# Performance work log

Measured on AMD Instinct MI355X. Metric: run time of the kernel, lower is better.

## Reference

```python
import jax, jax.numpy as jnp
import numpy as np

N = 500_000          # number of tree nodes
K = 8                # attributes per group
ROWS, COLS = 2048, 4096   # image size; P = ROWS*COLS pixels


def _build_euler_tour(n, seed=0):
    """Random tree (parent[i] < i, parent[0] = 0) + real DFS Euler tour with a
    single timer incremented on both entry (tpre) and exit (tpost)."""
    rng = np.random.default_rng(seed)
    parent = np.zeros(n, dtype=np.int64)
    if n > 1:
        parent[1:] = np.floor(rng.random(n - 1) * np.arange(1, n)).astype(np.int64)
    counts = np.bincount(parent[1:], minlength=n)
    starts = np.zeros(n, dtype=np.int64)
    starts[1:] = np.cumsum(counts)[:-1]
    child_order = np.argsort(parent[1:], kind='stable') + 1  # children grouped by parent
    tpre = np.empty(n, dtype=np.int64)
    tpost = np.empty(n, dtype=np.int64)
    next_child = starts.copy()
    ends = starts + counts
    stack = np.empty(n, dtype=np.int64)
    sp = 0
    stack[0] = 0
    timer = 0
    tpre[0] = timer; timer += 1
    while sp >= 0:
        u = stack[sp]
        if next_child[u] < ends[u]:
            v = child_order[next_child[u]]
            next_child[u] += 1
            sp += 1
            stack[sp] = v
            tpre[v] = timer; timer += 1
        else:
            tpost[u] = timer; timer += 1
            sp -= 1
    return tpre, tpost


def setup_inputs() -> dict:
    key = jax.random.key(0)
    k1, k2, k3, k4 = jax.random.split(key, 4)
    tpre_np, tpost_np = _build_euler_tour(N)
    weight = jax.random.normal(k1, (K,), dtype=jnp.float32) * 0.1
    bias = jnp.zeros((1,), dtype=jnp.float32)
    residues = jax.random.normal(k2, (N,), dtype=jnp.float32)
    attrs2d = jax.random.uniform(k3, (N, K), dtype=jnp.float32)
    node_of_pixel = jax.random.randint(k4, (ROWS * COLS,), 0, N)
    return {
        'weight': weight,
        'bias': bias,
        'residues': residues,
        'attrs2d': attrs2d,
        'tpre': jnp.asarray(tpre_np),
        'tpost': jnp.asarray(tpost_np),
        'node_of_pixel': node_of_pixel,
        'numRows': ROWS,
        'numCols': COLS,
    }


def reference(weight, bias, residues, attrs2d, tpre, tpost, node_of_pixel, numRows, numCols):
    beta_f = 1.0  # module default; clamp_logits=False
    # logits = attrs2d @ w + b ; filtered residues per node
    logits = attrs2d @ weight + bias[0]                     # (N,)
    sig = jax.nn.sigmoid(beta_f * logits)                   # (N,)
    filtered = residues * sig                                # (N,)
    # implicit J.T @ filtered via Euler-tour scatter + prefix scan
    T = 2 * tpre.shape[0]                                    # tpost.max()+1 for a full DFS tour
    delta = (jnp.zeros((T,), dtype=filtered.dtype)
             .at[tpre].add(filtered)
             .at[tpost].add(-filtered))
    y_cumsum = jnp.cumsum(delta)                             # (2N,)
    y = y_cumsum[tpre[node_of_pixel]]                        # (P,) gather per pixel
    return y.reshape(numRows, numCols)
```

## Files before the change

### kernel.cpp

```cpp
#include <hip/hip_runtime.h>

#define SCAN_THREADS 256
#define EPT 8
#define CHUNK (SCAN_THREADS * EPT)

__global__ void k1_filter_scatter(const float* __restrict__ attrs,
                                  const float* __restrict__ weight,
                                  const float* __restrict__ bias,
                                  const float* __restrict__ residues,
                                  const int* __restrict__ tpre,
                                  const int* __restrict__ tpost,
                                  float* __restrict__ delta,
                                  int N) {
    int u = blockIdx.x * blockDim.x + threadIdx.x;
    if (u >= N) return;
    const float4* a4 = (const float4*)(attrs + (size_t)u * 8);
    float4 a0 = a4[0];
    float4 a1 = a4[1];
    float4 w0 = ((const float4*)weight)[0];
    float4 w1 = ((const float4*)weight)[1];
    float logit = a0.x * w0.x + a0.y * w0.y + a0.z * w0.z + a0.w * w0.w +
                  a1.x * w1.x + a1.y * w1.y + a1.z * w1.z + a1.w * w1.w +
                  bias[0];
    float sig = 1.0f / (1.0f + __expf(-logit));
    float f = residues[u] * sig;
    delta[tpre[u]]  =  f;
    delta[tpost[u]] = -f;
}

__global__ void k2_partials(const float* __restrict__ delta,
                            float* __restrict__ partials, int T) {
    __shared__ float sdata[SCAN_THREADS / 64];
    int base = blockIdx.x * CHUNK + threadIdx.x * EPT;
    float s = 0.0f;
    if (base + EPT <= T) {
        float4 v0 = *(const float4*)(delta + base);
        float4 v1 = *(const float4*)(delta + base + 4);
        s = v0.x + v0.y + v0.z + v0.w + v1.x + v1.y + v1.z + v1.w;
    } else {
        for (int i = 0; i < EPT; ++i)
            if (base + i < T) s += delta[base + i];
    }
    for (int d = 32; d > 0; d >>= 1) s += __shfl_down(s, d, 64);
    int lane = threadIdx.x & 63, wid = threadIdx.x >> 6;
    if (lane == 0) sdata[wid] = s;
    __syncthreads();
    if (threadIdx.x == 0) {
        float tot = 0.0f;
        for (int i = 0; i < SCAN_THREADS / 64; ++i) tot += sdata[i];
        partials[blockIdx.x] = tot;
    }
}

__global__ void k3_scan_partials(const float* __restrict__ partials,
                                 float* __restrict__ offsets, int numChunks) {
    int lane = threadIdx.x;
    int ppl = (numChunks + 63) >> 6;
    float s = 0.0f;
    for (int i = 0; i < ppl; ++i) {
        int idx = lane * ppl + i;
        if (idx < numChunks) s += partials[idx];
    }
    float x = s;
    for (int d = 1; d < 64; d <<= 1) {
        float y = __shfl_up(x, d, 64);
        if (lane >= d) x += y;
    }
    float run = x - s;
    for (int i = 0; i < ppl; ++i) {
        int idx = lane * ppl + i;
        if (idx < numChunks) { offsets[idx] = run; run += partials[idx]; }
    }
}

__global__ void k4_scan_chunks(float* __restrict__ data,
                               const float* __restrict__ offsets, int T) {
    __shared__ float wavesums[SCAN_THREADS / 64];
    int base = blockIdx.x * CHUNK + threadIdx.x * EPT;
    float v[EPT];
    bool full = (base + EPT <= T);
    if (full) {
        float4 v0 = *(const float4*)(data + base);
        float4 v1 = *(const float4*)(data + base + 4);
        v[0] = v0.x; v[1] = v0.y; v[2] = v0.z; v[3] = v0.w;
        v[4] = v1.x; v[5] = v1.y; v[6] = v1.z; v[7] = v1.w;
    } else {
        for (int i = 0; i < EPT; ++i)
            v[i] = (base + i < T) ? data[base + i] : 0.0f;
    }
    float run = 0.0f;
    for (int i = 0; i < EPT; ++i) { run += v[i]; v[i] = run; }
    float tot = run;
    int lane = threadIdx.x & 63, wid = threadIdx.x >> 6;
    float x = tot;
    for (int d = 1; d < 64; d <<= 1) {
        float y = __shfl_up(x, d, 64);
        if (lane >= d) x += y;
    }
    if (lane == 63) wavesums[wid] = x;
    __syncthreads();
    float woff = 0.0f;
    for (int i = 0; i < wid; ++i) woff += wavesums[i];
    float add = (x - tot) + woff + offsets[blockIdx.x];
    if (full) {
        float4 o0 = make_float4(v[0] + add, v[1] + add, v[2] + add, v[3] + add);
        float4 o1 = make_float4(v[4] + add, v[5] + add, v[6] + add, v[7] + add);
        *(float4*)(data + base)     = o0;
        *(float4*)(data + base + 4) = o1;
    } else {
        for (int i = 0; i < EPT; ++i)
            if (base + i < T) data[base + i] = v[i] + add;
    }
}

__global__ void k5_node_values(const float* __restrict__ ycum,
                               const int* __restrict__ tpre,
                               float* __restrict__ vnode, int N) {
    int u = blockIdx.x * blockDim.x + threadIdx.x;
    if (u < N) vnode[u] = ycum[tpre[u]];
}

__global__ void k6_gather(const float* __restrict__ vnode,
                          const int* __restrict__ nop,
                          float* __restrict__ out, int P) {
    int i = (blockIdx.x * blockDim.x + threadIdx.x) * 4;
    if (i + 4 <= P) {
        int4 n = *(const int4*)(nop + i);
        float4 o = make_float4(vnode[n.x], vnode[n.y], vnode[n.z], vnode[n.w]);
        *(float4*)(out + i) = o;
    } else {
        for (; i < P; ++i) out[i] = vnode[nop[i]];
    }
}

__global__ void k6_direct(const float* __restrict__ ycum,
                          const int* __restrict__ tpre,
                          const int* __restrict__ nop,
                          float* __restrict__ out, int P) {
    int i = (blockIdx.x * blockDim.x + threadIdx.x) * 4;
    if (i + 4 <= P) {
        int4 n = *(const int4*)(nop + i);
        float4 o = make_float4(ycum[tpre[n.x]], ycum[tpre[n.y]],
                               ycum[tpre[n.z]], ycum[tpre[n.w]]);
        *(float4*)(out + i) = o;
    } else {
        for (; i < P; ++i) out[i] = ycum[tpre[nop[i]]];
    }
}

extern "C" void kernel_launch(void* const* d_in, const int* in_sizes, int n_in,
                              void* d_out, int out_size, void* d_ws, size_t ws_size,
                              hipStream_t stream) {
    const float* weight   = (const float*)d_in[0];
    const float* bias     = (const float*)d_in[1];
    const float* residues = (const float*)d_in[2];
    const float* attrs    = (const float*)d_in[3];
    const int*   tpre     = (const int*)d_in[4];
    const int*   tpost    = (const int*)d_in[5];
    const int*   nop      = (const int*)d_in[6];
    float* out = (float*)d_out;

    const int N = in_sizes[2];
    const int T = 2 * N;
    const int P = out_size;
    const int numChunks = (T + CHUNK - 1) / CHUNK;

    size_t needFull = (size_t)(T + N + 2 * 1024) * sizeof(float);
    size_t needMid  = (size_t)(N + 2 * 1024) * sizeof(float);

    float* delta;
    float* vnode    = nullptr;
    float* partials;
    float* offsets;
    bool useVnode = true;

    if (ws_size >= needFull) {
        delta    = (float*)d_ws;
        vnode    = delta + T;
        partials = vnode + N;
        offsets  = partials + 1024;
    } else if (ws_size >= needMid) {
        delta    = out;
        vnode    = (float*)d_ws;
        partials = vnode + N;
        offsets  = partials + 1024;
    } else {
        delta    = out;
        partials = (float*)d_ws;
        offsets  = partials + 1024;
        useVnode = false;
    }

    k1_filter_scatter<<<(N + 255) / 256, 256, 0, stream>>>(
        attrs, weight, bias, residues, tpre, tpost, delta, N);
    k2_partials<<<numChunks, SCAN_THREADS, 0, stream>>>(delta, partials, T);
    k3_scan_partials<<<1, 64, 0, stream>>>(partials, offsets, numChunks);
    k4_scan_chunks<<<numChunks, SCAN_THREADS, 0, stream>>>(delta, offsets, T);

    int gatherBlocks = (P / 4 + 255) / 256;
    if (useVnode) {
        k5_node_values<<<(N + 255) / 256, 256, 0, stream>>>(delta, tpre, vnode, N);
        k6_gather<<<gatherBlocks, 256, 0, stream>>>(vnode, nop, out, P);
    } else {
        k6_direct<<<gatherBlocks, 256, 0, stream>>>(delta, tpre, nop, out, P);
    }
}
```

Before: 166.3 us.

## Replace three-kernel scan with single-pass decoupled-lookback scan and widen per-thread work

The separate partials, partial-scan and chunk-scan kernels become one single-pass scan. Each tile takes a dynamic ticket, publishes its aggregate or inclusive prefix as a flag-packed 64-bit word, and looks back over earlier tiles one wavefront at a time. This removes two launches and one full extra pass over the delta buffer. In exchange it adds a memset for the control state and spin-waits on earlier tiles. The filter/scatter, node-value and pixel-gather kernels are also widened to 4, 8 and 16 elements per thread, with nontemporal loads and stores on the streaming arrays, to raise memory-level parallelism.

```diff
diff --git a/kernel.cpp b/kernel.cpp
--- a/kernel.cpp
+++ b/kernel.cpp
@@ -3,6 +3,13 @@
 #define SCAN_THREADS 256
 #define EPT 8
 #define CHUNK (SCAN_THREADS * EPT)
+
+typedef int   v4i __attribute__((ext_vector_type(4)));
+typedef float v4f __attribute__((ext_vector_type(4)));
+
+__device__ inline unsigned long long pack_sf(float v, unsigned flag) {
+    return ((unsigned long long)flag << 32) | (unsigned long long)__float_as_uint(v);
+}
 
 __global__ void k1_filter_scatter(const float* __restrict__ attrs,
                                   const float* __restrict__ weight,
@@ -12,101 +19,133 @@
                                   const int* __restrict__ tpost,
                                   float* __restrict__ delta,
                                   int N) {
-    int u = blockIdx.x * blockDim.x + threadIdx.x;
-    if (u >= N) return;
-    const float4* a4 = (const float4*)(attrs + (size_t)u * 8);
-    float4 a0 = a4[0];
-    float4 a1 = a4[1];
-    float4 w0 = ((const float4*)weight)[0];
-    float4 w1 = ((const float4*)weight)[1];
-    float logit = a0.x * w0.x + a0.y * w0.y + a0.z * w0.z + a0.w * w0.w +
-                  a1.x * w1.x + a1.y * w1.y + a1.z * w1.z + a1.w * w1.w +
-                  bias[0];
-    float sig = 1.0f / (1.0f + __expf(-logit));
-    float f = residues[u] * sig;
-    delta[tpre[u]]  =  f;
-    delta[tpost[u]] = -f;
-}
-
-__global__ void k2_partials(const float* __restrict__ delta,
-                            float* __restrict__ partials, int T) {
-    __shared__ float sdata[SCAN_THREADS / 64];
-    int base = blockIdx.x * CHUNK + threadIdx.x * EPT;
-    float s = 0.0f;
-    if (base + EPT <= T) {
-        float4 v0 = *(const float4*)(delta + base);
-        float4 v1 = *(const float4*)(delta + base + 4);
-        s = v0.x + v0.y + v0.z + v0.w + v1.x + v1.y + v1.z + v1.w;
-    } else {
-        for (int i = 0; i < EPT; ++i)
-            if (base + i < T) s += delta[base + i];
-    }
-    for (int d = 32; d > 0; d >>= 1) s += __shfl_down(s, d, 64);
+    int u0 = (blockIdx.x * blockDim.x + threadIdx.x) * 4;
+    v4f w0 = *(const v4f*)weight;
+    v4f w1 = *(const v4f*)(weight + 4);
+    float b = bias[0];
+    if (u0 + 4 <= N) {
+        v4f r  = __builtin_nontemporal_load((const v4f*)(residues + u0));
+        v4i pre  = *(const v4i*)(tpre + u0);
+        v4i post = __builtin_nontemporal_load((const v4i*)(tpost + u0));
+        float f[4];
+        #pragma unroll
+        for (int j = 0; j < 4; ++j) {
+            v4f a0 = __builtin_nontemporal_load((const v4f*)(attrs + (size_t)(u0 + j) * 8));
+            v4f a1 = __builtin_nontemporal_load((const v4f*)(attrs + (size_t)(u0 + j) * 8 + 4));
+            float logit = a0.x*w0.x + a0.y*w0.y + a0.z*w0.z + a0.w*w0.w +
+                          a1.x*w1.x + a1.y*w1.y + a1.z*w1.z + a1.w*w1.w + b;
+            float sig = 1.0f / (1.0f + __expf(-logit));
+            f[j] = ((const float*)&r)[j] * sig;
+        }
+        delta[pre.x]  =  f[0]; delta[pre.y]  =  f[1];
+        delta[pre.z]  =  f[2]; delta[pre.w]  =  f[3];
+        delta[post.x] = -f[0]; delta[post.y] = -f[1];
+        delta[post.z] = -f[2]; delta[post.w] = -f[3];
+    } else {
+        for (int u = u0; u < N; ++u) {
+            float logit = b;
+            #pragma unroll
+            for (int k = 0; k < 8; ++k) logit += attrs[(size_t)u * 8 + k] * weight[k];
+            float sig = 1.0f / (1.0f + __expf(-logit));
+            float f = residues[u] * sig;
+            delta[tpre[u]]  =  f;
+            delta[tpost[u]] = -f;
+        }
+    }
+}
+
+__global__ void scan_onepass(float* __restrict__ data,
+                             unsigned long long* __restrict__ state,
+                             int* __restrict__ ticket, int T) {
+    __shared__ int s_tile;
+    __shared__ float s_carry;
+    __shared__ float wavesums[SCAN_THREADS / 64];
+    if (threadIdx.x == 0) s_tile = atomicAdd(ticket, 1);
+    __syncthreads();
+    const int tile = s_tile;
+    const int base = tile * CHUNK + threadIdx.x * EPT;
+
+    float v[EPT];
+    bool full = (base + EPT <= T);
+    if (full) {
+        v4f a = *(const v4f*)(data + base);
+        v4f c = *(const v4f*)(data + base + 4);
+        v[0]=a.x; v[1]=a.y; v[2]=a.z; v[3]=a.w;
+        v[4]=c.x; v[5]=c.y; v[6]=c.z; v[7]=c.w;
+    } else {
+        for (int i = 0; i < EPT; ++i) v[i] = (base + i < T) ? data[base + i] : 0.0f;
+    }
+    float run = 0.0f;
+    #pragma unroll
+    for (int i = 0; i < EPT; ++i) { run += v[i]; v[i] = run; }
+    float tot = run;
+
     int lane = threadIdx.x & 63, wid = threadIdx.x >> 6;
-    if (lane == 0) sdata[wid] = s;
-    __syncthreads();
-    if (threadIdx.x == 0) {
-        float tot = 0.0f;
-        for (int i = 0; i < SCAN_THREADS / 64; ++i) tot += sdata[i];
-        partials[blockIdx.x] = tot;
-    }
-}
-
-__global__ void k3_scan_partials(const float* __restrict__ partials,
-                                 float* __restrict__ offsets, int numChunks) {
-    int lane = threadIdx.x;
-    int ppl = (numChunks + 63) >> 6;
-    float s = 0.0f;
-    for (int i = 0; i < ppl; ++i) {
-        int idx = lane * ppl + i;
-        if (idx < numChunks) s += partials[idx];
-    }
-    float x = s;
+    float x = tot;
+    #pragma unroll
     for (int d = 1; d < 64; d <<= 1) {
         float y = __shfl_up(x, d, 64);
         if (lane >= d) x += y;
     }
-    float run = x - s;
-    for (int i = 0; i < ppl; ++i) {
-        int idx = lane * ppl + i;
-        if (idx < numChunks) { offsets[idx] = run; run += partials[idx]; }
-    }
-}
-
-__global__ void k4_scan_chunks(float* __restrict__ data,
-                               const float* __restrict__ offsets, int T) {
-    __shared__ float wavesums[SCAN_THREADS / 64];
-    int base = blockIdx.x * CHUNK + threadIdx.x * EPT;
-    float v[EPT];
-    bool full = (base + EPT <= T);
-    if (full) {
-        float4 v0 = *(const float4*)(data + base);
-        float4 v1 = *(const float4*)(data + base + 4);
-        v[0] = v0.x; v[1] = v0.y; v[2] = v0.z; v[3] = v0.w;
-        v[4] = v1.x; v[5] = v1.y; v[6] = v1.z; v[7] = v1.w;
-    } else {
-        for (int i = 0; i < EPT; ++i)
-            v[i] = (base + i < T) ? data[base + i] : 0.0f;
-    }
-    float run = 0.0f;
-    for (int i = 0; i < EPT; ++i) { run += v[i]; v[i] = run; }
-    float tot = run;
-    int lane = threadIdx.x & 63, wid = threadIdx.x >> 6;
-    float x = tot;
-    for (int d = 1; d < 64; d <<= 1) {
-        float y = __shfl_up(x, d, 64);
-        if (lane >= d) x += y;
-    }
     if (lane == 63) wavesums[wid] = x;
     __syncthreads();
-    float woff = 0.0f;
-    for (int i = 0; i < wid; ++i) woff += wavesums[i];
-    float add = (x - tot) + woff + offsets[blockIdx.x];
+    float agg = 0.0f, woff = 0.0f;
+    #pragma unroll
+    for (int i = 0; i < SCAN_THREADS / 64; ++i) {
+        if (i < wid) woff += wavesums[i];
+        agg += wavesums[i];
+    }
+    float texcl = (x - tot) + woff;
+
+    if (threadIdx.x == 0) {
+        unsigned long long p = pack_sf(agg, (tile == 0) ? 2u : 1u);
+        __hip_atomic_store(&state[tile], p, __ATOMIC_RELEASE, __HIP_MEMORY_SCOPE_AGENT);
+    }
+
+    if (wid == 0) {
+        float carry = 0.0f;
+        if (tile > 0) {
+            int offset = 0;
+            while (true) {
+                int idx = tile - 1 - offset - lane;
+                float val; int flg;
+                if (idx >= 0) {
+                    unsigned long long p;
+                    do {
+                        p = __hip_atomic_load(&state[idx], __ATOMIC_ACQUIRE,
+                                              __HIP_MEMORY_SCOPE_AGENT);
+                        flg = (int)(p >> 32);
+                    } while (flg == 0);
+                    val = __uint_as_float((unsigned)(p & 0xffffffffu));
+                } else { val = 0.0f; flg = 2; }
+                unsigned long long m2 = __ballot(flg == 2);
+                int L = (m2 != 0) ? (__ffsll((unsigned long long)m2) - 1) : 64;
+                float contrib = (lane <= L) ? val : 0.0f;
+                #pragma unroll
+                for (int d = 32; d > 0; d >>= 1) contrib += __shfl_down(contrib, d, 64);
+                contrib = __shfl(contrib, 0, 64);
+                carry += contrib;
+                if (m2 != 0) break;
+                offset += 64;
+            }
+        }
+        if (lane == 0) {
+            s_carry = carry;
+            if (tile > 0) {
+                unsigned long long p = pack_sf(carry + agg, 2u);
+                __hip_atomic_store(&state[tile], p, __ATOMIC_RELEASE,
+                                   __HIP_MEMORY_SCOPE_AGENT);
+            }
+        }
+    }
+    __syncthreads();
+    float add = s_carry + texcl;
+
     if (full) {
-        float4 o0 = make_float4(v[0] + add, v[1] + add, v[2] + add, v[3] + add);
-        float4 o1 = make_float4(v[4] + add, v[5] + add, v[6] + add, v[7] + add);
-        *(float4*)(data + base)     = o0;
-        *(float4*)(data + base + 4) = o1;
+        v4f o0 = { v[0]+add, v[1]+add, v[2]+add, v[3]+add };
+        v4f o1 = { v[4]+add, v[5]+add, v[6]+add, v[7]+add };
+        *(v4f*)(data + base)     = o0;
+        *(v4f*)(data + base + 4) = o1;
     } else {
         for (int i = 0; i < EPT; ++i)
             if (base + i < T) data[base + i] = v[i] + add;
@@ -116,18 +155,36 @@
 __global__ void k5_node_values(const float* __restrict__ ycum,
                                const int* __restrict__ tpre,
                                float* __restrict__ vnode, int N) {
-    int u = blockIdx.x * blockDim.x + threadIdx.x;
-    if (u < N) vnode[u] = ycum[tpre[u]];
+    int u0 = (blockIdx.x * blockDim.x + threadIdx.x) * 8;
+    if (u0 + 8 <= N) {
+        v4i t0 = *(const v4i*)(tpre + u0);
+        v4i t1 = *(const v4i*)(tpre + u0 + 4);
+        v4f o0 = { ycum[t0.x], ycum[t0.y], ycum[t0.z], ycum[t0.w] };
+        v4f o1 = { ycum[t1.x], ycum[t1.y], ycum[t1.z], ycum[t1.w] };
+        *(v4f*)(vnode + u0)     = o0;
+        *(v4f*)(vnode + u0 + 4) = o1;
+    } else {
+        for (int u = u0; u < N; ++u) vnode[u] = ycum[tpre[u]];
+    }
 }
 
 __global__ void k6_gather(const float* __restrict__ vnode,
                           const int* __restrict__ nop,
                           float* __restrict__ out, int P) {
-    int i = (blockIdx.x * blockDim.x + threadIdx.x) * 4;
-    if (i + 4 <= P) {
-        int4 n = *(const int4*)(nop + i);
-        float4 o = make_float4(vnode[n.x], vnode[n.y], vnode[n.z], vnode[n.w]);
-        *(float4*)(out + i) = o;
+    int i = (blockIdx.x * blockDim.x + threadIdx.x) * 16;
+    if (i + 16 <= P) {
+        v4i n0 = __builtin_nontemporal_load((const v4i*)(nop + i));
+        v4i n1 = __builtin_nontemporal_load((const v4i*)(nop + i + 4));
+        v4i n2 = __builtin_nontemporal_load((const v4i*)(nop + i + 8));
+        v4i n3 = __builtin_nontemporal_load((const v4i*)(nop + i + 12));
+        v4f o0 = { vnode[n0.x], vnode[n0.y], vnode[n0.z], vnode[n0.w] };
+        v4f o1 = { vnode[n1.x], vnode[n1.y], vnode[n1.z], vnode[n1.w] };
+        v4f o2 = { vnode[n2.x], vnode[n2.y], vnode[n2.z], vnode[n2.w] };
+        v4f o3 = { vnode[n3.x], vnode[n3.y], vnode[n3.z], vnode[n3.w] };
+        __builtin_nontemporal_store(o0, (v4f*)(out + i));
+        __builtin_nontemporal_store(o1, (v4f*)(out + i + 4));
+        __builtin_nontemporal_store(o2, (v4f*)(out + i + 8));
+        __builtin_nontemporal_store(o3, (v4f*)(out + i + 12));
     } else {
         for (; i < P; ++i) out[i] = vnode[nop[i]];
     }
@@ -139,10 +196,9 @@
                           float* __restrict__ out, int P) {
     int i = (blockIdx.x * blockDim.x + threadIdx.x) * 4;
     if (i + 4 <= P) {
-        int4 n = *(const int4*)(nop + i);
-        float4 o = make_float4(ycum[tpre[n.x]], ycum[tpre[n.y]],
-                               ycum[tpre[n.z]], ycum[tpre[n.w]]);
-        *(float4*)(out + i) = o;
+        v4i n = *(const v4i*)(nop + i);
+        v4f o = { ycum[tpre[n.x]], ycum[tpre[n.y]], ycum[tpre[n.z]], ycum[tpre[n.w]] };
+        *(v4f*)(out + i) = o;
     } else {
         for (; i < P; ++i) out[i] = ycum[tpre[nop[i]]];
     }
@@ -165,43 +221,42 @@
     const int P = out_size;
     const int numChunks = (T + CHUNK - 1) / CHUNK;
 
-    size_t needFull = (size_t)(T + N + 2 * 1024) * sizeof(float);
-    size_t needMid  = (size_t)(N + 2 * 1024) * sizeof(float);
+    const size_t ctrlBytes = 1024 * sizeof(unsigned long long) + 64;
+    size_t needFull = (size_t)(T + N) * sizeof(float) + ctrlBytes;
+    size_t needMid  = (size_t)N * sizeof(float) + ctrlBytes;
 
     float* delta;
-    float* vnode    = nullptr;
-    float* partials;
-    float* offsets;
+    float* vnode = nullptr;
+    unsigned long long* state;
     bool useVnode = true;
 
     if (ws_size >= needFull) {
-        delta    = (float*)d_ws;
-        vnode    = delta + T;
-        partials = vnode + N;
-        offsets  = partials + 1024;
+        delta = (float*)d_ws;
+        vnode = delta + T;
+        state = (unsigned long long*)(vnode + N);
     } else if (ws_size >= needMid) {
-        delta    = out;
-        vnode    = (float*)d_ws;
-        partials = vnode + N;
-        offsets  = partials + 1024;
-    } else {
-        delta    = out;
-        partials = (float*)d_ws;
-        offsets  = partials + 1024;
+        delta = out;
+        vnode = (float*)d_ws;
+        state = (unsigned long long*)(vnode + N);
+    } else {
+        delta = out;
+        state = (unsigned long long*)d_ws;
         useVnode = false;
     }
-
-    k1_filter_scatter<<<(N + 255) / 256, 256, 0, stream>>>(
+    int* ticket = (int*)(state + 1024);
+
+    hipMemsetAsync(state, 0, ctrlBytes, stream);
+
+    k1_filter_scatter<<<(N / 4 + 255) / 256, 256, 0, stream>>>(
         attrs, weight, bias, residues, tpre, tpost, delta, N);
-    k2_partials<<<numChunks, SCAN_THREADS, 0, stream>>>(delta, partials, T);
-    k3_scan_partials<<<1, 64, 0, stream>>>(partials, offsets, numChunks);
-    k4_scan_chunks<<<numChunks, SCAN_THREADS, 0, stream>>>(delta, offsets, T);
-
-    int gatherBlocks = (P / 4 + 255) / 256;
+    scan_onepass<<<numChunks, SCAN_THREADS, 0, stream>>>(delta, state, ticket, T);
+
     if (useVnode) {
-        k5_node_values<<<(N + 255) / 256, 256, 0, stream>>>(delta, tpre, vnode, N);
+        k5_node_values<<<(N / 8 + 255) / 256, 256, 0, stream>>>(delta, tpre, vnode, N);
+        int gatherBlocks = (P / 16 + 255) / 256;
         k6_gather<<<gatherBlocks, 256, 0, stream>>>(vnode, nop, out, P);
     } else {
+        int gatherBlocks = (P / 4 + 255) / 256;
         k6_direct<<<gatherBlocks, 256, 0, stream>>>(delta, tpre, nop, out, P);
     }
 }
```

After: 224.8 us. 35.1% more time.
